# Performance work log

Measured on AMD Instinct MI355X. Metric: run time of the kernel, lower is better.

Reference implementation:

```python
import jax, jax.numpy as jnp
import numpy as np

B, I, H = 32768, 512, 512


def _uniform(key, shape, fan_in):
    bound = 1.0 / np.sqrt(fan_in)
    return jax.random.uniform(key, shape, jnp.float32, -bound, bound)


def setup_inputs() -> dict:
    key = jax.random.key(0)
    ks = jax.random.split(key, 16)
    inp = {
        "x": jax.random.normal(ks[0], (B, I), jnp.float32),
        "h": jax.random.normal(ks[1], (B, H), jnp.float32),
        "c_prev": jax.random.normal(ks[2], (B, H), jnp.float32),
        # weights stored as [in, out] so we apply x @ W (transpose of torch layout)
        "Wxi": _uniform(ks[3], (I, H), I), "bxi": _uniform(ks[4], (H,), I),
        "Whi": _uniform(ks[5], (H, H), H),
        "Wxf": _uniform(ks[6], (I, H), I), "bxf": _uniform(ks[7], (H,), I),
        "Whf": _uniform(ks[8], (H, H), H),
        "Wxc": _uniform(ks[9], (I, H), I), "bxc": _uniform(ks[10], (H,), I),
        "Whc": _uniform(ks[11], (H, H), H),
        "Wxo": _uniform(ks[12], (I, H), I), "bxo": _uniform(ks[13], (H,), I),
        "Who": _uniform(ks[14], (H, H), H),
    }
    return inp


def reference(x, h, c_prev, Wxi, bxi, Whi, Wxf, bxf, Whf, Wxc, bxc, Whc, Wxo, bxo, Who):
    # Faithful to source: peephole (w_c) projections are dead code; the
    # forget path f*c_prev is computed then discarded, so c_next = i * tanh(.)
    i = jax.nn.sigmoid(x @ Wxi + bxi + h @ Whi)            # input gate
    f = jax.nn.sigmoid(x @ Wxf + bxf + h @ Whf)            # computed, unused (as in source)
    c_next = i * jnp.tanh(x @ Wxc + bxc + h @ Whc)         # NOTE: no f*c_prev term (source bug)
    o = jax.nn.sigmoid(x @ Wxo + bxo + h @ Who)            # output gate
    h_next = o * jnp.tanh(c_next)
    del f, c_prev  # unused, matching the original module's effective math
    return (h_next, c_next)
```

## Files before the change

### kernel.cpp

```cpp
#include <hip/hip_runtime.h>
#include <hip/hip_bf16.h>


typedef unsigned short u16;
typedef u16 u16x8 __attribute__((ext_vector_type(8)));
typedef __bf16 bf16x8 __attribute__((ext_vector_type(8)));
typedef float f32x4 __attribute__((ext_vector_type(4)));

#define B_DIM 32768
#define H_DIM 512
#define K_DIM 1024
#define BH_ELEMS (B_DIM * H_DIM)
#define U_ELEMS ((long)B_DIM * K_DIM)
#define WT_BYTES (3u * 512u * 1024u * 2u)
#define U_BYTES ((size_t)U_ELEMS * 2u)

#define GLOBAL_AS(p) ((__attribute__((address_space(1))) void*)(p))
#define LDS_AS(p)    ((__attribute__((address_space(3))) void*)(p))

__device__ __forceinline__ float bf2f(u16 u) {
    unsigned v = ((unsigned)u) << 16;
    float f;
    __builtin_memcpy(&f, &v, 4);
    return f;
}

__device__ __forceinline__ u16 f2bf16u(float f) {
    __hip_bfloat16 b = __float2bfloat16(f);
    u16 u;
    __builtin_memcpy(&u, &b, 2);
    return u;
}

__device__ __forceinline__ float fast_sigmoid(float x) {
    return 1.0f / (1.0f + __expf(-x));
}

__device__ __forceinline__ float fast_tanh(float x) {
    float e = __expf(-2.0f * fabsf(x));
    float r = (1.0f - e) / (1.0f + e);
    return x < 0.0f ? -r : r;
}

__device__ __forceinline__ void gload16(const u16* g, u16* l) {
    __builtin_amdgcn_global_load_lds(GLOBAL_AS((u16*)g), LDS_AS(l), 16, 0, 0);
}

__global__ void probe_dtype(const unsigned* __restrict__ x, int* __restrict__ flag) {
    const int lane = threadIdx.x;
    const unsigned lo = x[lane] & 0xFFFFu;
    const unsigned e = (lo >> 7) & 0xFFu;
    const bool sane = (e >= 100u && e <= 140u) || (lo == 0u);
    const unsigned long long m = __ballot(sane);
    if (lane == 0) *flag = (__popcll(m) >= 48) ? 1 : 0;
}

__global__ void pack_weights(const void* __restrict__ Wxi, const void* __restrict__ Whi,
                             const void* __restrict__ Wxc, const void* __restrict__ Whc,
                             const void* __restrict__ Wxo, const void* __restrict__ Who,
                             const int* __restrict__ flag, u16* __restrict__ Wt)
{
    __shared__ u16 tile[32][33];
    const bool isbf = (*flag != 0);
    const int g = blockIdx.z >> 1, half = blockIdx.z & 1;
    const void* src;
    if (g == 0)      src = half ? Whi : Wxi;
    else if (g == 1) src = half ? Whc : Wxc;
    else             src = half ? Who : Wxo;
    const int kk = blockIdx.y * 32, nn = blockIdx.x * 32;
    const int tx = threadIdx.x, ty = threadIdx.y;
    if (isbf) {
        const u16* s = (const u16*)src;
#pragma unroll
        for (int i2 = 0; i2 < 4; ++i2)
            tile[ty + 8 * i2][tx] = s[(kk + ty + 8 * i2) * 512 + nn + tx];
    } else {
        const float* s = (const float*)src;
#pragma unroll
        for (int i2 = 0; i2 < 4; ++i2)
            tile[ty + 8 * i2][tx] = f2bf16u(s[(kk + ty + 8 * i2) * 512 + nn + tx]);
    }
    __syncthreads();
#pragma unroll
    for (int i2 = 0; i2 < 4; ++i2)
        Wt[(long)g * 524288 + (long)(nn + ty + 8 * i2) * 1024 + half * 512 + kk + tx]
            = tile[tx][ty + 8 * i2];
}

__global__ __launch_bounds__(256) void pack_u(
    const void* __restrict__ x, const void* __restrict__ h,
    const int* __restrict__ flag, u16* __restrict__ U)
{
    const bool isbf = (*flag != 0);
    const long stride = (long)gridDim.x * blockDim.x;
    for (long t = (long)blockIdx.x * blockDim.x + threadIdx.x;
         t < (U_ELEMS >> 3); t += stride) {
        const long e = t << 3;
        const int r = (int)(e >> 10);
        const int k = (int)(e & 1023);
        const void* src = (k < 512) ? x : h;
        const long so = (long)r * 512 + (k & 511);
        u16x8 o;
        if (isbf) {
            o = *(const u16x8*)((const u16*)src + so);
        } else {
            const float* s = (const float*)src + so;
            f32x4 p0 = *(const f32x4*)s;
            f32x4 p1 = *(const f32x4*)(s + 4);
#pragma unroll
            for (int j = 0; j < 4; ++j) {
                o[j] = f2bf16u(p0[j]);
                o[4 + j] = f2bf16u(p1[j]);
            }
        }
        *(u16x8*)(U + e) = o;
    }
}

__global__ __launch_bounds__(256, 2) void lstm_gemm_v2(
    const u16* __restrict__ U, const u16* __restrict__ Wt,
    const void* __restrict__ bxi, const void* __restrict__ bxc,
    const void* __restrict__ bxo, const int* __restrict__ flag,
    void* __restrict__ out)
{
    __shared__ __align__(16) u16 As[128 * 64];
    __shared__ __align__(16) u16 Bs[3 * 64 * 64];

    const bool isbf = (*flag != 0);
    const int tid    = threadIdx.x;
    const int lane   = tid & 63;
    const int wave   = tid >> 6;
    const int wave_m = wave & 1;
    const int wave_n = wave >> 1;

    const int swz = (blockIdx.x & 7) * 256 + (blockIdx.x >> 3);
    const int m0 = (swz >> 3) * 128;
    const int n0 = (swz & 7) * 64;

    const int srow = lane >> 3;
    const int sk2  = (lane & 7) ^ srow;
    const u16* a_src[4];
#pragma unroll
    for (int j = 0; j < 4; ++j) {
        const int ca = wave * 4 + j;
        a_src[j] = U + (long)(m0 + ca * 8 + srow) * 1024 + sk2 * 8;
    }
    const u16* b_src[6];
#pragma unroll
    for (int q = 0; q < 6; ++q) {
        const int cb = q * 4 + wave;
        const int g = cb >> 3;
        const int nrow = (cb & 7) * 8 + srow;
        b_src[q] = Wt + (long)g * 524288 + (long)(n0 + nrow) * 1024 + sk2 * 8;
    }

    int a_off[4];
#pragma unroll
    for (int mt = 0; mt < 4; ++mt) {
        const int row = wave_m * 64 + mt * 16 + (lane & 15);
        const int p = (lane >> 4) ^ (row & 7);
        a_off[mt] = row * 64 + p * 8;
    }
    int b_off[3][2];
#pragma unroll
    for (int g = 0; g < 3; ++g)
#pragma unroll
        for (int nt = 0; nt < 2; ++nt) {
            const int row = wave_n * 32 + nt * 16 + (lane & 15);
            const int p = (lane >> 4) ^ (row & 7);
            b_off[g][nt] = g * 4096 + row * 64 + p * 8;
        }

    f32x4 acc[3][4][2];
    const f32x4 zero = {0.f, 0.f, 0.f, 0.f};
#pragma unroll
    for (int g = 0; g < 3; ++g)
#pragma unroll
        for (int mt = 0; mt < 4; ++mt)
#pragma unroll
            for (int nt = 0; nt < 2; ++nt)
                acc[g][mt][nt] = zero;

    for (int k0 = 0; k0 < K_DIM; k0 += 64) {
        __syncthreads();
#pragma unroll
        for (int j = 0; j < 4; ++j)
            gload16(a_src[j] + k0, &As[(wave * 4 + j) * 512]);
#pragma unroll
        for (int q = 0; q < 6; ++q)
            gload16(b_src[q] + k0, &Bs[(q * 4 + wave) * 512]);
        __syncthreads();

#pragma unroll
        for (int kk = 0; kk < 2; ++kk) {
            const int kx = kk * 32;
            bf16x8 af[4];
#pragma unroll
            for (int mt = 0; mt < 4; ++mt)
                af[mt] = *(const bf16x8*)&As[a_off[mt] ^ kx];
            bf16x8 bfr[3][2];
#pragma unroll
            for (int g = 0; g < 3; ++g)
#pragma unroll
                for (int nt = 0; nt < 2; ++nt)
                    bfr[g][nt] = *(const bf16x8*)&Bs[b_off[g][nt] ^ kx];
#pragma unroll
            for (int g = 0; g < 3; ++g)
#pragma unroll
                for (int mt = 0; mt < 4; ++mt)
#pragma unroll
                    for (int nt = 0; nt < 2; ++nt)
                        acc[g][mt][nt] = __builtin_amdgcn_mfma_f32_16x16x32_bf16(
                            af[mt], bfr[g][nt], acc[g][mt][nt], 0, 0, 0);
        }
    }

    const int colbase = n0 + wave_n * 32 + (lane & 15);
    float bi[2], bc[2], bo[2];
#pragma unroll
    for (int nt = 0; nt < 2; ++nt) {
        const int col = colbase + nt * 16;
        if (isbf) {
            bi[nt] = bf2f(((const u16*)bxi)[col]);
            bc[nt] = bf2f(((const u16*)bxc)[col]);
            bo[nt] = bf2f(((const u16*)bxo)[col]);
        } else {
            bi[nt] = ((const float*)bxi)[col];
            bc[nt] = ((const float*)bxc)[col];
            bo[nt] = ((const float*)bxo)[col];
        }
    }

    const int rowbase = m0 + wave_m * 64 + (lane >> 4) * 4;
#pragma unroll
    for (int mt = 0; mt < 4; ++mt)
#pragma unroll
        for (int nt = 0; nt < 2; ++nt)
#pragma unroll
            for (int r = 0; r < 4; ++r) {
                const int row = rowbase + mt * 16 + r;
                const int col = colbase + nt * 16;
                const float iv = fast_sigmoid(acc[0][mt][nt][r] + bi[nt]);
                const float cv = iv * fast_tanh(acc[1][mt][nt][r] + bc[nt]);
                const float ov = fast_sigmoid(acc[2][mt][nt][r] + bo[nt]);
                const float hv = ov * fast_tanh(cv);
                const long idx = (long)row * 512 + col;
                if (isbf) {
                    ((u16*)out)[idx]            = f2bf16u(hv);
                    ((u16*)out)[BH_ELEMS + idx] = f2bf16u(cv);
                } else {
                    ((float*)out)[idx]            = hv;
                    ((float*)out)[BH_ELEMS + idx] = cv;
                }
            }
}

__global__ __launch_bounds__(256, 2) void lstm_gemm_fb(
    const void* __restrict__ x, const void* __restrict__ h,
    const u16* __restrict__ Wt,
    const void* __restrict__ bxi, const void* __restrict__ bxc,
    const void* __restrict__ bxo, const int* __restrict__ flag,
    void* __restrict__ out)
{
    __shared__ __align__(16) u16 As[128 * 32];
    __shared__ __align__(16) u16 Bs[3 * 64 * 32];

    const bool isbf = (*flag != 0);
    const int tid    = threadIdx.x;
    const int lane   = tid & 63;
    const int wave   = tid >> 6;
    const int wave_m = wave & 1;
    const int wave_n = wave >> 1;
    const int m0 = blockIdx.y * 128;
    const int n0 = blockIdx.x * 64;

    const int trow = tid >> 2, tkc = (tid & 3) * 8;
    const long a_g0 = (long)(m0 + trow)      * 512 + tkc;
    const long a_g1 = (long)(m0 + 64 + trow) * 512 + tkc;
    const int  a_l0 = tid * 8;
    const int  a_l1 = 2048 + tid * 8;
    long b_g[3];
#pragma unroll
    for (int q = 0; q < 3; ++q)
        b_g[q] = (long)q * 524288 + (long)(n0 + trow) * 1024 + tkc;

    int a_ld[4];
#pragma unroll
    for (int mt = 0; mt < 4; ++mt)
        a_ld[mt] = (wave_m * 64 + mt * 16 + (lane & 15)) * 32 + (lane >> 4) * 8;
    int b_ld[3][2];
#pragma unroll
    for (int g = 0; g < 3; ++g)
#pragma unroll
        for (int nt = 0; nt < 2; ++nt)
            b_ld[g][nt] = g * 2048 + (wave_n * 32 + nt * 16 + (lane & 15)) * 32 + (lane >> 4) * 8;

    f32x4 acc[3][4][2];
    const f32x4 zero = {0.f, 0.f, 0.f, 0.f};
#pragma unroll
    for (int g = 0; g < 3; ++g)
#pragma unroll
        for (int mt = 0; mt < 4; ++mt)
#pragma unroll
            for (int nt = 0; nt < 2; ++nt)
                acc[g][mt][nt] = zero;

    for (int k0 = 0; k0 < K_DIM; k0 += 32) {
        const void* src = (k0 < 512) ? x : h;
        const long kadj = (k0 < 512) ? k0 : (k0 - 512);

        bf16x8 av0, av1, bv[3];
        if (isbf) {
            const u16* s = (const u16*)src + kadj;
            u16x8 t0 = *(const u16x8*)(s + a_g0);
            u16x8 t1 = *(const u16x8*)(s + a_g1);
            __builtin_memcpy(&av0, &t0, 16);
            __builtin_memcpy(&av1, &t1, 16);
        } else {
            const float* s = (const float*)src + kadj;
            f32x4 p0 = *(const f32x4*)(s + a_g0);
            f32x4 p1 = *(const f32x4*)(s + a_g0 + 4);
            f32x4 q0 = *(const f32x4*)(s + a_g1);
            f32x4 q1 = *(const f32x4*)(s + a_g1 + 4);
#pragma unroll
            for (int j = 0; j < 4; ++j) {
                av0[j] = (__bf16)p0[j]; av0[4 + j] = (__bf16)p1[j];
                av1[j] = (__bf16)q0[j]; av1[4 + j] = (__bf16)q1[j];
            }
        }
#pragma unroll
        for (int q = 0; q < 3; ++q) {
            u16x8 t = *(const u16x8*)(Wt + b_g[q] + k0);
            __builtin_memcpy(&bv[q], &t, 16);
        }

        __syncthreads();
        *(bf16x8*)&As[a_l0] = av0;
        *(bf16x8*)&As[a_l1] = av1;
#pragma unroll
        for (int q = 0; q < 3; ++q)
            *(bf16x8*)&Bs[q * 2048 + tid * 8] = bv[q];
        __syncthreads();

        bf16x8 af[4];
#pragma unroll
        for (int mt = 0; mt < 4; ++mt)
            af[mt] = *(const bf16x8*)&As[a_ld[mt]];
        bf16x8 bfr[3][2];
#pragma unroll
        for (int g = 0; g < 3; ++g)
#pragma unroll
            for (int nt = 0; nt < 2; ++nt)
                bfr[g][nt] = *(const bf16x8*)&Bs[b_ld[g][nt]];

#pragma unroll
        for (int g = 0; g < 3; ++g)
#pragma unroll
            for (int mt = 0; mt < 4; ++mt)
#pragma unroll
            for (int nt = 0; nt < 2; ++nt)
                acc[g][mt][nt] = __builtin_amdgcn_mfma_f32_16x16x32_bf16(
                    af[mt], bfr[g][nt], acc[g][mt][nt], 0, 0, 0);
    }

    const int colbase = n0 + wave_n * 32 + (lane & 15);
    float bi[2], bc[2], bo[2];
#pragma unroll
    for (int nt = 0; nt < 2; ++nt) {
        const int col = colbase + nt * 16;
        if (isbf) {
            bi[nt] = bf2f(((const u16*)bxi)[col]);
            bc[nt] = bf2f(((const u16*)bxc)[col]);
            bo[nt] = bf2f(((const u16*)bxo)[col]);
        } else {
            bi[nt] = ((const float*)bxi)[col];
            bc[nt] = ((const float*)bxc)[col];
            bo[nt] = ((const float*)bxo)[col];
        }
    }

    const int rowbase = m0 + wave_m * 64 + (lane >> 4) * 4;
#pragma unroll
    for (int mt = 0; mt < 4; ++mt)
#pragma unroll
        for (int nt = 0; nt < 2; ++nt)
#pragma unroll
            for (int r = 0; r < 4; ++r) {
                const int row = rowbase + mt * 16 + r;
                const int col = colbase + nt * 16;
                const float iv = fast_sigmoid(acc[0][mt][nt][r] + bi[nt]);
                const float cv = iv * fast_tanh(acc[1][mt][nt][r] + bc[nt]);
                const float ov = fast_sigmoid(acc[2][mt][nt][r] + bo[nt]);
                const float hv = ov * fast_tanh(cv);
                const long idx = (long)row * 512 + col;
                if (isbf) {
                    ((u16*)out)[idx]            = f2bf16u(hv);
                    ((u16*)out)[BH_ELEMS + idx] = f2bf16u(cv);
                } else {
                    ((float*)out)[idx]            = hv;
                    ((float*)out)[BH_ELEMS + idx] = cv;
                }
            }
}

extern "C" void kernel_launch(void* const* d_in, const int* in_sizes, int n_in,
                              void* d_out, int out_size, void* d_ws, size_t ws_size,
                              hipStream_t stream) {
    const void* x   = d_in[0];
    const void* h   = d_in[1];
    const void* Wxi = d_in[3];
    const void* bxi = d_in[4];
    const void* Whi = d_in[5];
    const void* Wxc = d_in[9];
    const void* bxc = d_in[10];
    const void* Whc = d_in[11];
    const void* Wxo = d_in[12];
    const void* bxo = d_in[13];
    const void* Who = d_in[14];

    int* flag = (int*)d_ws;
    u16* Wt   = (u16*)((char*)d_ws + 256);
    const size_t need = 256 + (size_t)WT_BYTES + U_BYTES;

    probe_dtype<<<1, 64, 0, stream>>>((const unsigned*)x, flag);
    pack_weights<<<dim3(16, 16, 6), dim3(32, 8), 0, stream>>>(
        Wxi, Whi, Wxc, Whc, Wxo, Who, flag, Wt);

    if (ws_size >= need) {
        u16* U = (u16*)((char*)d_ws + 256 + WT_BYTES);
        pack_u<<<dim3(4096), dim3(256), 0, stream>>>(x, h, flag, U);
        lstm_gemm_v2<<<dim3(2048), dim3(256), 0, stream>>>(
            U, Wt, bxi, bxc, bxo, flag, d_out);
    } else {
        lstm_gemm_fb<<<dim3(8, 256), dim3(256), 0, stream>>>(
            x, h, Wt, bxi, bxc, bxo, flag, d_out);
    }
}
```

Baseline: 390.7 us.

## Double-buffer GEMM LDS tiles, fuse prep kernels, inline dtype probe

The main GEMM now double-buffers its A/B LDS tiles so global-to-LDS loads for the next K step are issued before the MFMAs on the current one, and the loop is fully unrolled. The dtype probe, weight packing and activation packing are merged into one prep launch, with each block deriving the dtype flag itself instead of reading a workspace flag. Sigmoid and tanh divisions are replaced with hardware reciprocal. Doubling LDS per block (about 80KB) may cut occupancy below the intended two blocks per CU, and the fast reciprocal slightly changes numerics.

```diff
diff --git a/kernel.cpp b/kernel.cpp
--- a/kernel.cpp
+++ b/kernel.cpp
@@ -12,7 +12,7 @@
 #define K_DIM 1024
 #define BH_ELEMS (B_DIM * H_DIM)
 #define U_ELEMS ((long)B_DIM * K_DIM)
-#define WT_BYTES (3u * 512u * 1024u * 2u)
+#define WT_BYTES ((size_t)(3u * 512u * 1024u * 2u))
 #define U_BYTES ((size_t)U_ELEMS * 2u)
 
 #define GLOBAL_AS(p) ((__attribute__((address_space(1))) void*)(p))
@@ -32,102 +32,107 @@
     return u;
 }
 
+__device__ __forceinline__ float fast_rcp(float x) {
+    return __builtin_amdgcn_rcpf(x);
+}
+
 __device__ __forceinline__ float fast_sigmoid(float x) {
-    return 1.0f / (1.0f + __expf(-x));
+    return fast_rcp(1.0f + __expf(-x));
 }
 
 __device__ __forceinline__ float fast_tanh(float x) {
     float e = __expf(-2.0f * fabsf(x));
-    float r = (1.0f - e) / (1.0f + e);
+    float r = (1.0f - e) * fast_rcp(1.0f + e);
     return x < 0.0f ? -r : r;
+}
+
+__device__ __forceinline__ bool derive_isbf(const unsigned* __restrict__ x, int tid) {
+    const unsigned lo = x[tid & 63] & 0xFFFFu;
+    const unsigned e = (lo >> 7) & 0xFFu;
+    const bool sane = (e >= 100u && e <= 140u) || (lo == 0u);
+    return __popcll(__ballot(sane)) >= 48;
 }
 
 __device__ __forceinline__ void gload16(const u16* g, u16* l) {
     __builtin_amdgcn_global_load_lds(GLOBAL_AS((u16*)g), LDS_AS(l), 16, 0, 0);
 }
 
-__global__ void probe_dtype(const unsigned* __restrict__ x, int* __restrict__ flag) {
-    const int lane = threadIdx.x;
-    const unsigned lo = x[lane] & 0xFFFFu;
-    const unsigned e = (lo >> 7) & 0xFFu;
-    const bool sane = (e >= 100u && e <= 140u) || (lo == 0u);
-    const unsigned long long m = __ballot(sane);
-    if (lane == 0) *flag = (__popcll(m) >= 48) ? 1 : 0;
-}
-
-__global__ void pack_weights(const void* __restrict__ Wxi, const void* __restrict__ Whi,
-                             const void* __restrict__ Wxc, const void* __restrict__ Whc,
-                             const void* __restrict__ Wxo, const void* __restrict__ Who,
-                             const int* __restrict__ flag, u16* __restrict__ Wt)
+__global__ __launch_bounds__(256) void prep(
+    const void* __restrict__ x, const void* __restrict__ h,
+    const void* __restrict__ Wxi, const void* __restrict__ Whi,
+    const void* __restrict__ Wxc, const void* __restrict__ Whc,
+    const void* __restrict__ Wxo, const void* __restrict__ Who,
+    u16* __restrict__ Wt, u16* __restrict__ U)
 {
     __shared__ u16 tile[32][33];
-    const bool isbf = (*flag != 0);
-    const int g = blockIdx.z >> 1, half = blockIdx.z & 1;
-    const void* src;
-    if (g == 0)      src = half ? Whi : Wxi;
-    else if (g == 1) src = half ? Whc : Wxc;
-    else             src = half ? Who : Wxo;
-    const int kk = blockIdx.y * 32, nn = blockIdx.x * 32;
-    const int tx = threadIdx.x, ty = threadIdx.y;
-    if (isbf) {
-        const u16* s = (const u16*)src;
+    const int tid = threadIdx.x;
+    const bool isbf = derive_isbf((const unsigned*)x, tid);
+    const int bid = blockIdx.x;
+
+    if (bid < 1536) {
+        const int bz = bid >> 8, rem = bid & 255;
+        const int by = rem >> 4, bx = rem & 15;
+        const int g = bz >> 1, half = bz & 1;
+        const void* src;
+        if (g == 0)      src = half ? Whi : Wxi;
+        else if (g == 1) src = half ? Whc : Wxc;
+        else             src = half ? Who : Wxo;
+        const int kk = by * 32, nn = bx * 32;
+        const int tx = tid & 31, ty = tid >> 5;
+        if (isbf) {
+            const u16* s = (const u16*)src;
+#pragma unroll
+            for (int i2 = 0; i2 < 4; ++i2)
+                tile[ty + 8 * i2][tx] = s[(kk + ty + 8 * i2) * 512 + nn + tx];
+        } else {
+            const float* s = (const float*)src;
+#pragma unroll
+            for (int i2 = 0; i2 < 4; ++i2)
+                tile[ty + 8 * i2][tx] = f2bf16u(s[(kk + ty + 8 * i2) * 512 + nn + tx]);
+        }
+        __syncthreads();
 #pragma unroll
         for (int i2 = 0; i2 < 4; ++i2)
-            tile[ty + 8 * i2][tx] = s[(kk + ty + 8 * i2) * 512 + nn + tx];
+            Wt[(long)g * 524288 + (long)(nn + ty + 8 * i2) * 1024 + half * 512 + kk + tx]
+                = tile[tx][ty + 8 * i2];
     } else {
-        const float* s = (const float*)src;
-#pragma unroll
-        for (int i2 = 0; i2 < 4; ++i2)
-            tile[ty + 8 * i2][tx] = f2bf16u(s[(kk + ty + 8 * i2) * 512 + nn + tx]);
-    }
-    __syncthreads();
-#pragma unroll
-    for (int i2 = 0; i2 < 4; ++i2)
-        Wt[(long)g * 524288 + (long)(nn + ty + 8 * i2) * 1024 + half * 512 + kk + tx]
-            = tile[tx][ty + 8 * i2];
-}
-
-__global__ __launch_bounds__(256) void pack_u(
-    const void* __restrict__ x, const void* __restrict__ h,
-    const int* __restrict__ flag, u16* __restrict__ U)
-{
-    const bool isbf = (*flag != 0);
-    const long stride = (long)gridDim.x * blockDim.x;
-    for (long t = (long)blockIdx.x * blockDim.x + threadIdx.x;
-         t < (U_ELEMS >> 3); t += stride) {
-        const long e = t << 3;
-        const int r = (int)(e >> 10);
-        const int k = (int)(e & 1023);
-        const void* src = (k < 512) ? x : h;
-        const long so = (long)r * 512 + (k & 511);
-        u16x8 o;
-        if (isbf) {
-            o = *(const u16x8*)((const u16*)src + so);
-        } else {
-            const float* s = (const float*)src + so;
-            f32x4 p0 = *(const f32x4*)s;
-            f32x4 p1 = *(const f32x4*)(s + 4);
-#pragma unroll
-            for (int j = 0; j < 4; ++j) {
-                o[j] = f2bf16u(p0[j]);
-                o[4 + j] = f2bf16u(p1[j]);
+        const long stride = 4096L * 256L;
+        for (long t = (long)(bid - 1536) * 256 + tid;
+             t < (U_ELEMS >> 3); t += stride) {
+            const long e = t << 3;
+            const int r = (int)(e >> 10);
+            const int k = (int)(e & 1023);
+            const void* src = (k < 512) ? x : h;
+            const long so = (long)r * 512 + (k & 511);
+            u16x8 o;
+            if (isbf) {
+                o = *(const u16x8*)((const u16*)src + so);
+            } else {
+                const float* s = (const float*)src + so;
+                f32x4 p0 = *(const f32x4*)s;
+                f32x4 p1 = *(const f32x4*)(s + 4);
+#pragma unroll
+                for (int j = 0; j < 4; ++j) {
+                    o[j] = f2bf16u(p0[j]);
+                    o[4 + j] = f2bf16u(p1[j]);
+                }
             }
-        }
-        *(u16x8*)(U + e) = o;
-    }
-}
-
-__global__ __launch_bounds__(256, 2) void lstm_gemm_v2(
+            *(u16x8*)(U + e) = o;
+        }
+    }
+}
+
+__global__ __launch_bounds__(256, 2) void lstm_gemm_v3(
+    const void* __restrict__ x,
     const u16* __restrict__ U, const u16* __restrict__ Wt,
     const void* __restrict__ bxi, const void* __restrict__ bxc,
-    const void* __restrict__ bxo, const int* __restrict__ flag,
-    void* __restrict__ out)
+    const void* __restrict__ bxo, void* __restrict__ out)
 {
-    __shared__ __align__(16) u16 As[128 * 64];
-    __shared__ __align__(16) u16 Bs[3 * 64 * 64];
-
-    const bool isbf = (*flag != 0);
+    __shared__ __align__(16) u16 As[2][128 * 64];
+    __shared__ __align__(16) u16 Bs[2][3 * 64 * 64];
+
     const int tid    = threadIdx.x;
+    const bool isbf  = derive_isbf((const unsigned*)x, tid);
     const int lane   = tid & 63;
     const int wave   = tid >> 6;
     const int wave_m = wave & 1;
@@ -154,6 +159,15 @@
         b_src[q] = Wt + (long)g * 524288 + (long)(n0 + nrow) * 1024 + sk2 * 8;
     }
 
+#define STAGE_TILE(bi, kofs) do {                                         \
+    _Pragma("unroll")                                                     \
+    for (int j_ = 0; j_ < 4; ++j_)                                        \
+        gload16(a_src[j_] + (kofs), &As[bi][(wave * 4 + j_) * 512]);      \
+    _Pragma("unroll")                                                     \
+    for (int q_ = 0; q_ < 6; ++q_)                                        \
+        gload16(b_src[q_] + (kofs), &Bs[bi][(q_ * 4 + wave) * 512]);      \
+} while (0)
+
     int a_off[4];
 #pragma unroll
     for (int mt = 0; mt < 4; ++mt) {
@@ -181,15 +195,12 @@
             for (int nt = 0; nt < 2; ++nt)
                 acc[g][mt][nt] = zero;
 
-    for (int k0 = 0; k0 < K_DIM; k0 += 64) {
-        __syncthreads();
-#pragma unroll
-        for (int j = 0; j < 4; ++j)
-            gload16(a_src[j] + k0, &As[(wave * 4 + j) * 512]);
-#pragma unroll
-        for (int q = 0; q < 6; ++q)
-            gload16(b_src[q] + k0, &Bs[(q * 4 + wave) * 512]);
-        __syncthreads();
+    STAGE_TILE(0, 0);
+    __syncthreads();
+#pragma unroll
+    for (int t = 0; t < 16; ++t) {
+        const int cur = t & 1;
+        if (t < 15) STAGE_TILE(cur ^ 1, (t + 1) * 64);
 
 #pragma unroll
         for (int kk = 0; kk < 2; ++kk) {
@@ -197,13 +208,14 @@
             bf16x8 af[4];
 #pragma unroll
             for (int mt = 0; mt < 4; ++mt)
-                af[mt] = *(const bf16x8*)&As[a_off[mt] ^ kx];
+                af[mt] = *(const bf16x8*)&As[cur][a_off[mt] ^ kx];
             bf16x8 bfr[3][2];
 #pragma unroll
             for (int g = 0; g < 3; ++g)
 #pragma unroll
                 for (int nt = 0; nt < 2; ++nt)
-                    bfr[g][nt] = *(const bf16x8*)&Bs[b_off[g][nt] ^ kx];
+                    bfr[g][nt] = *(const bf16x8*)&Bs[cur][b_off[g][nt] ^ kx];
+
 #pragma unroll
             for (int g = 0; g < 3; ++g)
 #pragma unroll
@@ -213,7 +225,9 @@
                         acc[g][mt][nt] = __builtin_amdgcn_mfma_f32_16x16x32_bf16(
                             af[mt], bfr[g][nt], acc[g][mt][nt], 0, 0, 0);
         }
-    }
+        if (t < 15) __syncthreads();
+    }
+#undef STAGE_TILE
 
     const int colbase = n0 + wave_n * 32 + (lane & 15);
     float bi[2], bc[2], bo[2];
@@ -259,14 +273,13 @@
     const void* __restrict__ x, const void* __restrict__ h,
     const u16* __restrict__ Wt,
     const void* __restrict__ bxi, const void* __restrict__ bxc,
-    const void* __restrict__ bxo, const int* __restrict__ flag,
-    void* __restrict__ out)
+    const void* __restrict__ bxo, void* __restrict__ out)
 {
     __shared__ __align__(16) u16 As[128 * 32];
     __shared__ __align__(16) u16 Bs[3 * 64 * 32];
 
-    const bool isbf = (*flag != 0);
     const int tid    = threadIdx.x;
+    const bool isbf  = derive_isbf((const unsigned*)x, tid);
     const int lane   = tid & 63;
     const int wave   = tid >> 6;
     const int wave_m = wave & 1;
@@ -418,21 +431,19 @@
     const void* bxo = d_in[13];
     const void* Who = d_in[14];
 
-    int* flag = (int*)d_ws;
-    u16* Wt   = (u16*)((char*)d_ws + 256);
-    const size_t need = 256 + (size_t)WT_BYTES + U_BYTES;
-
-    probe_dtype<<<1, 64, 0, stream>>>((const unsigned*)x, flag);
-    pack_weights<<<dim3(16, 16, 6), dim3(32, 8), 0, stream>>>(
-        Wxi, Whi, Wxc, Whc, Wxo, Who, flag, Wt);
+    u16* Wt = (u16*)d_ws;
+    const size_t need = WT_BYTES + U_BYTES;
 
     if (ws_size >= need) {
-        u16* U = (u16*)((char*)d_ws + 256 + WT_BYTES);
-        pack_u<<<dim3(4096), dim3(256), 0, stream>>>(x, h, flag, U);
-        lstm_gemm_v2<<<dim3(2048), dim3(256), 0, stream>>>(
-            U, Wt, bxi, bxc, bxo, flag, d_out);
+        u16* U = (u16*)((char*)d_ws + WT_BYTES);
+        prep<<<dim3(1536 + 4096), dim3(256), 0, stream>>>(
+            x, h, Wxi, Whi, Wxc, Whc, Wxo, Who, Wt, U);
+        lstm_gemm_v3<<<dim3(2048), dim3(256), 0, stream>>>(
+            x, U, Wt, bxi, bxc, bxo, d_out);
     } else {
+        prep<<<dim3(1536), dim3(256), 0, stream>>>(
+            x, h, Wxi, Whi, Wxc, Whc, Wxo, Who, Wt, nullptr);
         lstm_gemm_fb<<<dim3(8, 256), dim3(256), 0, stream>>>(
-            x, h, Wt, bxi, bxc, bxo, flag, d_out);
-    }
-}
+            x, h, Wt, bxi, bxc, bxo, d_out);
+    }
+}
```

Result: faster. 380.6 us (-2.6%).
